# Kernel tuning notes

Hardware: AMD Instinct MI355X
Metric: run time of the kernel (lower is better)

## Reference

```python
import jax, jax.numpy as jnp
import numpy as np

DIM = 2048
N_HEADS = 32
N_KV_HEADS = 8
HEAD_DIM = DIM // N_HEADS
B, T = 2, 2048


def setup_inputs() -> dict:
    key = jax.random.key(0)
    ks = jax.random.split(key, 5)
    std = 0.02
    return {
        "x": jax.random.normal(ks[0], (B, T, DIM), dtype=jnp.float32),
        "wq": jax.random.normal(ks[1], (DIM, DIM), dtype=jnp.float32) * std,
        "wk": jax.random.normal(ks[2], (N_KV_HEADS * HEAD_DIM, DIM), dtype=jnp.float32) * std,
        "wv": jax.random.normal(ks[3], (N_KV_HEADS * HEAD_DIM, DIM), dtype=jnp.float32) * std,
        "wo": jax.random.normal(ks[4], (DIM, DIM), dtype=jnp.float32) * std,
    }


def _rope_tables(seq_len, head_dim, dtype):
    inv_freq = 1.0 / (10000.0 ** (jnp.arange(0, head_dim, 2, dtype=jnp.float32) / head_dim))
    t = jnp.arange(seq_len, dtype=jnp.float32)
    freqs = jnp.einsum("i,j->ij", t, inv_freq)          # [T, hd/2]
    emb = jnp.concatenate([freqs, freqs], axis=-1)       # [T, hd]
    return jnp.cos(emb).astype(dtype), jnp.sin(emb).astype(dtype)


def _rotate_half(x):
    h = x.shape[-1] // 2
    return jnp.concatenate([-x[..., h:], x[..., :h]], axis=-1)


def reference(x, wq, wk, wv, wo):
    Bc, Tc, C = x.shape
    q = (x @ wq.T).reshape(Bc, Tc, N_HEADS, HEAD_DIM).transpose(0, 2, 1, 3)      # [B,H,T,hd]
    k = (x @ wk.T).reshape(Bc, Tc, N_KV_HEADS, HEAD_DIM).transpose(0, 2, 1, 3)   # [B,Hk,T,hd]
    v = (x @ wv.T).reshape(Bc, Tc, N_KV_HEADS, HEAD_DIM).transpose(0, 2, 1, 3)

    cos, sin = _rope_tables(Tc, HEAD_DIM, x.dtype)  # [T,hd] broadcast over B,H
    q = q * cos + _rotate_half(q) * sin
    k = k * cos + _rotate_half(k) * sin

    rep = N_HEADS // N_KV_HEADS
    k = jnp.repeat(k, rep, axis=1)  # [B,H,T,hd]
    v = jnp.repeat(v, rep, axis=1)

    scale = 1.0 / np.sqrt(HEAD_DIM)
    scores = jnp.einsum("bhqd,bhkd->bhqk", q, k) * scale   # [B,H,T,T]
    causal = jnp.triu(jnp.ones((Tc, Tc), dtype=bool), k=1)
    scores = jnp.where(causal, jnp.asarray(-jnp.inf, scores.dtype), scores)
    attn = jax.nn.softmax(scores, axis=-1)
    out = jnp.einsum("bhqk,bhkd->bhqd", attn, v)           # [B,H,T,hd]
    out = out.transpose(0, 2, 1, 3).reshape(Bc, Tc, C)
    return out @ wo.T
```

## Files before the change

### kernel.cpp

```cpp
#include <hip/hip_runtime.h>


typedef unsigned short u16;
typedef __attribute__((ext_vector_type(8))) short bf16x8;
typedef __attribute__((ext_vector_type(4))) float f32x4;
typedef __attribute__((ext_vector_type(4))) unsigned short u16x4;

constexpr int T_SEQ = 2048;
constexpr int DIMC  = 2048;
constexpr int NHEAD = 32;
constexpr int HDIM  = 64;
constexpr int KVDIM = 512;
constexpr int BATCH = 2;

__device__ __forceinline__ u16 f2bf(float f) {
    union { float f; unsigned int i; } v; v.f = f;
    unsigned int r = v.i + 0x7FFFu + ((v.i >> 16) & 1u);
    return (u16)(r >> 16);
}

__device__ __forceinline__ unsigned int pack2_bf16(float e0, float e1) {
    return __builtin_amdgcn_perm(__float_as_uint(e1), __float_as_uint(e0),
                                 0x07060302u);
}

typedef __attribute__((address_space(1))) unsigned int as1_uint;
typedef __attribute__((address_space(3))) unsigned int as3_uint;
__device__ __forceinline__ void glds16(const u16* g, u16* l) {
    __builtin_amdgcn_global_load_lds((as1_uint*)(u16*)g, (as3_uint*)l, 16, 0, 0);
}

__global__ __launch_bounds__(256) void cvt5(const float* __restrict__ x,
                                            const float* __restrict__ wq,
                                            const float* __restrict__ wk,
                                            const float* __restrict__ wv,
                                            const float* __restrict__ wo,
                                            u16* __restrict__ xb,  u16* __restrict__ wqb,
                                            u16* __restrict__ wkb, u16* __restrict__ wvb,
                                            u16* __restrict__ wob) {
    constexpr int E0 = BATCH * T_SEQ * DIMC;
    constexpr int E1 = E0 + DIMC * DIMC;
    constexpr int E2 = E1 + KVDIM * DIMC;
    constexpr int E3 = E2 + KVDIM * DIMC;
    constexpr int E4 = E3 + DIMC * DIMC;
    for (int i = (blockIdx.x * 256 + threadIdx.x) * 4; i < E4; i += gridDim.x * 1024) {
        const float* s; u16* d; int off;
        if (i < E0)      { s = x;  d = xb;  off = 0;  }
        else if (i < E1) { s = wq; d = wqb; off = E0; }
        else if (i < E2) { s = wk; d = wkb; off = E1; }
        else if (i < E3) { s = wv; d = wvb; off = E2; }
        else             { s = wo; d = wob; off = E3; }
        f32x4 v = *(const f32x4*)(s + (i - off));
        u16x4 o;
        #pragma unroll
        for (int e = 0; e < 4; ++e) o[e] = f2bf(v[e]);
        *(u16x4*)(d + (i - off)) = o;
    }
}

template <bool OUTF32>
__device__ __forceinline__ void gemm_core(const u16* __restrict__ A,
                                          const u16* __restrict__ W,
                                          void* __restrict__ Cv,
                                          int rowBase, int colBase,
                                          int N, int K, bool rope) {
    __shared__ __align__(16) u16 As[2 * 128 * 32];
    __shared__ __align__(16) u16 Bs[2 * 128 * 32];

    const int tid  = threadIdx.x;
    const int lane = tid & 63;
    const int w    = tid >> 6;
    const int quad = lane >> 4;
    const int ln   = lane & 15;
    const int wm = (w >> 1) * 64;
    const int wn = (w & 1) * 64;

    f32x4 acc[4][4] = {};

    const int srow = lane >> 2;
    const int scol = (lane & 3) * 8;
    const u16* aC0 = A + (size_t)(rowBase + w * 16 + srow) * K + scol;
    const u16* aC1 = A + (size_t)(rowBase + (w + 4) * 16 + srow) * K + scol;
    const u16* bC0 = W + (size_t)(colBase + w * 16 + srow) * K + scol;
    const u16* bC1 = W + (size_t)(colBase + (w + 4) * 16 + srow) * K + scol;
    u16* asl0 = As + w * 512;
    u16* asl1 = As + (w + 4) * 512;
    u16* bsl0 = Bs + w * 512;
    u16* bsl1 = Bs + (w + 4) * 512;

    for (int kk = 0; kk < K; kk += 64) {
        __syncthreads();
        glds16(aC0 + kk, asl0);
        glds16(aC1 + kk, asl1);
        glds16(bC0 + kk, bsl0);
        glds16(bC1 + kk, bsl1);
        glds16(aC0 + kk + 32, asl0 + 4096);
        glds16(aC1 + kk + 32, asl1 + 4096);
        glds16(bC0 + kk + 32, bsl0 + 4096);
        glds16(bC1 + kk + 32, bsl1 + 4096);
        __syncthreads();

        #pragma unroll
        for (int hp = 0; hp < 2; ++hp) {
            const u16* Ap = As + hp * 4096;
            const u16* Bp = Bs + hp * 4096;
            bf16x8 bw[4];
            #pragma unroll
            for (int j = 0; j < 4; ++j)
                bw[j] = *(const bf16x8*)(Bp + (wn + j * 16 + ln) * 32 + quad * 8);
            #pragma unroll
            for (int i = 0; i < 4; ++i) {
                bf16x8 af = *(const bf16x8*)(Ap + (wm + i * 16 + ln) * 32 + quad * 8);
                #pragma unroll
                for (int j = 0; j < 4; ++j)
                    acc[i][j] = __builtin_amdgcn_mfma_f32_16x16x32_bf16(af, bw[j], acc[i][j], 0, 0, 0);
            }
        }
    }

    if (rope) {
        #pragma unroll
        for (int j = 0; j < 2; ++j) {
            const int d = j * 16 + ln;
            const float invrev = exp2f(-(float)d * (13.287712379549449f / 32.0f))
                                 * 0.15915494309189535f;
            #pragma unroll
            for (int i = 0; i < 4; ++i) {
                #pragma unroll
                for (int r = 0; r < 4; ++r) {
                    const int t = (rowBase + wm + i * 16 + quad * 4 + r) & (T_SEQ - 1);
                    float rev = (float)t * invrev;
                    float fr = rev - floorf(rev);
                    float sn = __builtin_amdgcn_sinf(fr);
                    float cs = __builtin_amdgcn_cosf(fr);
                    float a0 = acc[i][j][r], a2 = acc[i][j + 2][r];
                    acc[i][j][r]     = a0 * cs - a2 * sn;
                    acc[i][j + 2][r] = a2 * cs + a0 * sn;
                }
            }
        }
    }

    #pragma unroll
    for (int i = 0; i < 4; ++i) {
        int mrow = rowBase + wm + i * 16 + quad * 4;
        #pragma unroll
        for (int j = 0; j < 4; ++j) {
            int n = colBase + wn + j * 16 + ln;
            #pragma unroll
            for (int r = 0; r < 4; ++r) {
                if constexpr (OUTF32)
                    ((float*)Cv)[(size_t)(mrow + r) * N + n] = acc[i][j][r];
                else
                    ((u16*)Cv)[(size_t)(mrow + r) * N + n] = f2bf(acc[i][j][r]);
            }
        }
    }
}

__global__ __launch_bounds__(256, 4) void qkv_gemm(const u16* __restrict__ xb,
                                                   const u16* __restrict__ wqb,
                                                   const u16* __restrict__ wkb,
                                                   const u16* __restrict__ wvb,
                                                   u16* __restrict__ Qb,
                                                   u16* __restrict__ Kb,
                                                   u16* __restrict__ Vb) {
    const int nb = blockIdx.x;
    const int rowBase = blockIdx.y * 128;
    const u16* W; u16* C; int colBase, N; bool rope;
    if (nb < 16)      { W = wqb; C = Qb; colBase = nb * 128;        N = DIMC;  rope = true; }
    else if (nb < 20) { W = wkb; C = Kb; colBase = (nb - 16) * 128; N = KVDIM; rope = true; }
    else              { W = wvb; C = Vb; colBase = (nb - 20) * 128; N = KVDIM; rope = false; }
    gemm_core<false>(xb, W, C, rowBase, colBase, N, DIMC, rope);
}

__global__ __launch_bounds__(256, 4) void gemm_out64(const u16* __restrict__ A,
                                                     const u16* __restrict__ W,
                                                     float* __restrict__ C) {
    __shared__ __align__(16) u16 As[2 * 128 * 32];
    __shared__ __align__(16) u16 Bs[2 * 64 * 32];

    const int tid  = threadIdx.x;
    const int lane = tid & 63;
    const int w    = tid >> 6;
    const int quad = lane >> 4;
    const int ln   = lane & 15;
    const int rowBase = blockIdx.y * 128;
    const int colBase = blockIdx.x * 64;
    const int wm = w * 32;
    constexpr int K = DIMC, N = DIMC;

    f32x4 acc[2][4] = {};

    const int srow = lane >> 2;
    const int scol = (lane & 3) * 8;
    const u16* aC0 = A + (size_t)(rowBase + w * 16 + srow) * K + scol;
    const u16* aC1 = A + (size_t)(rowBase + (w + 4) * 16 + srow) * K + scol;
    const u16* bC  = W + (size_t)(colBase + w * 16 + srow) * K + scol;
    u16* asl0 = As + w * 512;
    u16* asl1 = As + (w + 4) * 512;
    u16* bsl  = Bs + w * 512;

    for (int kk = 0; kk < K; kk += 64) {
        __syncthreads();
        glds16(aC0 + kk, asl0);
        glds16(aC1 + kk, asl1);
        glds16(bC  + kk, bsl);
        glds16(aC0 + kk + 32, asl0 + 4096);
        glds16(aC1 + kk + 32, asl1 + 4096);
        glds16(bC  + kk + 32, bsl + 2048);
        __syncthreads();

        #pragma unroll
        for (int hp = 0; hp < 2; ++hp) {
            const u16* Ap = As + hp * 4096;
            const u16* Bp = Bs + hp * 2048;
            bf16x8 bw[4];
            #pragma unroll
            for (int j = 0; j < 4; ++j)
                bw[j] = *(const bf16x8*)(Bp + (j * 16 + ln) * 32 + quad * 8);
            #pragma unroll
            for (int i = 0; i < 2; ++i) {
                bf16x8 af = *(const bf16x8*)(Ap + (wm + i * 16 + ln) * 32 + quad * 8);
                #pragma unroll
                for (int j = 0; j < 4; ++j)
                    acc[i][j] = __builtin_amdgcn_mfma_f32_16x16x32_bf16(af, bw[j], acc[i][j], 0, 0, 0);
            }
        }
    }

    #pragma unroll
    for (int i = 0; i < 2; ++i) {
        int mrow = rowBase + wm + i * 16 + quad * 4;
        #pragma unroll
        for (int j = 0; j < 4; ++j) {
            int n = colBase + j * 16 + ln;
            #pragma unroll
            for (int r = 0; r < 4; ++r)
                C[(size_t)(mrow + r) * N + n] = acc[i][j][r];
        }
    }
}

__global__ __launch_bounds__(256) void transpose_v(const u16* __restrict__ V,
                                                   u16* __restrict__ Vt) {
    __shared__ __align__(16) u16 tile[32][33];
    const int x = threadIdx.x & 31;
    const int y = threadIdx.x >> 5;
    const int tok0 = blockIdx.y * 32;
    const int c0   = blockIdx.x * 32;
    #pragma unroll
    for (int yy = 0; yy < 32; yy += 8)
        tile[y + yy][x] = V[(size_t)(tok0 + y + yy) * KVDIM + c0 + x];
    __syncthreads();
    const int b  = tok0 >> 11;
    const int t0 = tok0 & (T_SEQ - 1);
    #pragma unroll
    for (int yy = 0; yy < 32; yy += 8)
        Vt[(size_t)(b * KVDIM + c0 + y + yy) * T_SEQ + t0 + x] = tile[x][y + yy];
}

__global__ __launch_bounds__(256) void attn(const u16* __restrict__ Q,
                                            const u16* __restrict__ Kx,
                                            const u16* __restrict__ Vt,
                                            u16* __restrict__ O) {
    __shared__ __align__(16) u16 Ks[64][72];
    __shared__ __align__(16) u16 Vs[64][72];

    const int tid  = threadIdx.x;
    const int lane = tid & 63;
    const int w    = tid >> 6;
    const int quad = lane >> 4;
    const int ln   = lane & 15;
    const int h    = blockIdx.y;
    const int b    = blockIdx.z;
    const int kvh  = h >> 2;

    const int srow = tid >> 2;
    const int c    = tid & 3;
    const int scol = c * 16;
    const int vsb  = 32 * (c >> 1) + 4 * (c & 1);
    const u16* kbase = Kx + (size_t)(b * T_SEQ + srow) * KVDIM + kvh * HDIM + scol;
    const u16* vbase = Vt + (size_t)(b * KVDIM + kvh * HDIM + srow) * T_SEQ;

    const float K1 = 0.125f * 1.4426950408889634f;
    const float K2 = 8.0f * 1.4426950408889634f;

    #pragma unroll
    for (int phase = 0; phase < 2; ++phase) {
        const int qt = phase ? (31 - (int)blockIdx.x) : (int)blockIdx.x;
        const int qr0 = qt * 64 + w * 16;

        const u16* qp = Q + (size_t)(b * T_SEQ + qr0 + ln) * DIMC + h * HDIM + quad * 8;
        const bf16x8 bq0 = *(const bf16x8*)qp;
        const bf16x8 bq1 = *(const bf16x8*)(qp + 32);

        f32x4 o[4] = {};
        float lsum = 0.0f;

        for (int kt = 0; kt <= qt; ++kt) {
            const int k0 = kt * 64;
            __syncthreads();
            *(bf16x8*)&Ks[srow][scol]     = *(const bf16x8*)(kbase + (size_t)k0 * KVDIM);
            *(bf16x8*)&Ks[srow][scol + 8] = *(const bf16x8*)(kbase + (size_t)k0 * KVDIM + 8);
            {
                union { bf16x8 v; u16x4 h4[2]; } va, vb;
                va.v = *(const bf16x8*)(vbase + k0 + scol);
                vb.v = *(const bf16x8*)(vbase + k0 + scol + 8);
                *(u16x4*)&Vs[srow][vsb]      = va.h4[0];
                *(u16x4*)&Vs[srow][vsb + 8]  = va.h4[1];
                *(u16x4*)&Vs[srow][vsb + 16] = vb.h4[0];
                *(u16x4*)&Vs[srow][vsb + 24] = vb.h4[1];
            }
            __syncthreads();

            f32x4 s[4];
            #pragma unroll
            for (int st = 0; st < 4; ++st) {
                f32x4 z = {};
                s[st] = __builtin_amdgcn_mfma_f32_16x16x32_bf16(
                            *(const bf16x8*)&Ks[st * 16 + ln][quad * 8], bq0, z, 0, 0, 0);
                s[st] = __builtin_amdgcn_mfma_f32_16x16x32_bf16(
                            *(const bf16x8*)&Ks[st * 16 + ln][32 + quad * 8], bq1, s[st], 0, 0, 0);
            }

            unsigned int pk[8];
            if (kt != qt) {
                #pragma unroll
                for (int st = 0; st < 4; ++st) {
                    float e0 = exp2f(fmaf(s[st][0], K1, -K2));
                    float e1 = exp2f(fmaf(s[st][1], K1, -K2));
                    float e2 = exp2f(fmaf(s[st][2], K1, -K2));
                    float e3 = exp2f(fmaf(s[st][3], K1, -K2));
                    lsum += (e0 + e1) + (e2 + e3);
                    pk[2 * st]     = pack2_bf16(e0, e1);
                    pk[2 * st + 1] = pack2_bf16(e2, e3);
                }
            } else {
                const int thr = w * 16 + ln;
                #pragma unroll
                for (int st = 0; st < 4; ++st) {
                    float e[4];
                    #pragma unroll
                    for (int r = 0; r < 4; ++r) {
                        const int key = st * 16 + quad * 4 + r;
                        e[r] = (key > thr) ? 0.0f : exp2f(fmaf(s[st][r], K1, -K2));
                    }
                    lsum += (e[0] + e[1]) + (e[2] + e[3]);
                    pk[2 * st]     = pack2_bf16(e[0], e[1]);
                    pk[2 * st + 1] = pack2_bf16(e[2], e[3]);
                }
            }

            union { unsigned int u[4]; bf16x8 v; } a0, a1;
            a0.u[0] = pk[0]; a0.u[1] = pk[1]; a0.u[2] = pk[2]; a0.u[3] = pk[3];
            a1.u[0] = pk[4]; a1.u[1] = pk[5]; a1.u[2] = pk[6]; a1.u[3] = pk[7];

            #pragma unroll
            for (int t = 0; t < 4; ++t) {
                o[t] = __builtin_amdgcn_mfma_f32_16x16x32_bf16(
                           a0.v, *(const bf16x8*)&Vs[t * 16 + ln][quad * 8], o[t], 0, 0, 0);
                o[t] = __builtin_amdgcn_mfma_f32_16x16x32_bf16(
                           a1.v, *(const bf16x8*)&Vs[t * 16 + ln][32 + quad * 8], o[t], 0, 0, 0);
            }
        }

        float ls = lsum;
        ls += __shfl_xor(ls, 16);
        ls += __shfl_xor(ls, 32);
        #pragma unroll
        for (int r = 0; r < 4; ++r) {
            const float inv = 1.0f / __shfl(ls, quad * 4 + r);
            size_t obase = (size_t)(b * T_SEQ + qr0 + quad * 4 + r) * DIMC + h * HDIM;
            #pragma unroll
            for (int t = 0; t < 4; ++t)
                O[obase + t * 16 + ln] = f2bf(o[t][r] * inv);
        }
    }
}

extern "C" void kernel_launch(void* const* d_in, const int* in_sizes, int n_in,
                              void* d_out, int out_size, void* d_ws, size_t ws_size,
                              hipStream_t stream) {
    const float* x  = (const float*)d_in[0];
    const float* wq = (const float*)d_in[1];
    const float* wk = (const float*)d_in[2];
    const float* wv = (const float*)d_in[3];
    const float* wo = (const float*)d_in[4];
    float* out = (float*)d_out;

    char* ws = (char*)d_ws;
    constexpr size_t MB = 1024 * 1024;
    u16* Qb  = (u16*)(ws);
    u16* Kb  = (u16*)(ws + 16 * MB);
    u16* Vb  = (u16*)(ws + 20 * MB);
    u16* Vtb = (u16*)(ws + 24 * MB);
    u16* AOb = (u16*)(ws + 28 * MB);
    u16* xb  = AOb;
    u16* wqb = (u16*)(ws + 44 * MB);
    u16* wkb = (u16*)(ws + 52 * MB);
    u16* wvb = (u16*)(ws + 54 * MB);
    u16* wob = (u16*)(ws + 56 * MB);
    const int M = BATCH * T_SEQ;

    hipLaunchKernelGGL(cvt5, dim3(2048), dim3(256), 0, stream,
                       x, wq, wk, wv, wo, xb, wqb, wkb, wvb, wob);
    hipLaunchKernelGGL(qkv_gemm, dim3(24, M / 128), dim3(256), 0, stream,
                       xb, wqb, wkb, wvb, Qb, Kb, Vb);
    hipLaunchKernelGGL(transpose_v, dim3(KVDIM / 32, M / 32), dim3(256), 0, stream, Vb, Vtb);
    hipLaunchKernelGGL(attn, dim3(16, NHEAD, BATCH), dim3(256), 0, stream,
                       Qb, Kb, Vtb, AOb);
    hipLaunchKernelGGL(gemm_out64, dim3(DIMC / 64, M / 128), dim3(256), 0, stream,
                       AOb, wob, out);
}
```

Before: 316.7 us.

## Prefetch next K/V tile into registers and raise wave priority around MFMA

The attention loop now loads the next K and V tile from global memory into registers while the current tile is being computed, then writes them to shared memory at the start of the next iteration. The second __syncthreads is replaced by an explicit lgkmcnt wait plus s_barrier, so the barrier does not wait on the outstanding global prefetch loads. It also wraps the MFMA blocks in s_setprio to favour matrix issue. The goal is to hide global load latency behind compute, at the cost of extra VGPRs, which may reduce occupancy.

```diff
diff --git a/kernel.cpp b/kernel.cpp
--- a/kernel.cpp
+++ b/kernel.cpp
@@ -298,23 +298,38 @@
         f32x4 o[4] = {};
         float lsum = 0.0f;
 
+        bf16x8 kra = *(const bf16x8*)kbase;
+        bf16x8 krb = *(const bf16x8*)(kbase + 8);
+        bf16x8 vra = *(const bf16x8*)(vbase + scol);
+        bf16x8 vrb = *(const bf16x8*)(vbase + scol + 8);
+
         for (int kt = 0; kt <= qt; ++kt) {
-            const int k0 = kt * 64;
             __syncthreads();
-            *(bf16x8*)&Ks[srow][scol]     = *(const bf16x8*)(kbase + (size_t)k0 * KVDIM);
-            *(bf16x8*)&Ks[srow][scol + 8] = *(const bf16x8*)(kbase + (size_t)k0 * KVDIM + 8);
+
+            *(bf16x8*)&Ks[srow][scol]     = kra;
+            *(bf16x8*)&Ks[srow][scol + 8] = krb;
             {
-                union { bf16x8 v; u16x4 h4[2]; } va, vb;
-                va.v = *(const bf16x8*)(vbase + k0 + scol);
-                vb.v = *(const bf16x8*)(vbase + k0 + scol + 8);
-                *(u16x4*)&Vs[srow][vsb]      = va.h4[0];
-                *(u16x4*)&Vs[srow][vsb + 8]  = va.h4[1];
-                *(u16x4*)&Vs[srow][vsb + 16] = vb.h4[0];
-                *(u16x4*)&Vs[srow][vsb + 24] = vb.h4[1];
-            }
-            __syncthreads();
+                union { bf16x8 v; u16x4 h4[2]; } ua, ub;
+                ua.v = vra; ub.v = vrb;
+                *(u16x4*)&Vs[srow][vsb]      = ua.h4[0];
+                *(u16x4*)&Vs[srow][vsb + 8]  = ua.h4[1];
+                *(u16x4*)&Vs[srow][vsb + 16] = ub.h4[0];
+                *(u16x4*)&Vs[srow][vsb + 24] = ub.h4[1];
+            }
+
+            if (kt < qt) {
+                const size_t ko = (size_t)(kt + 1) * 64;
+                kra = *(const bf16x8*)(kbase + ko * KVDIM);
+                krb = *(const bf16x8*)(kbase + ko * KVDIM + 8);
+                vra = *(const bf16x8*)(vbase + ko + scol);
+                vrb = *(const bf16x8*)(vbase + ko + scol + 8);
+            }
+
+            __asm__ __volatile__("s_waitcnt lgkmcnt(0)" ::: "memory");
+            __builtin_amdgcn_s_barrier();
 
             f32x4 s[4];
+            __builtin_amdgcn_s_setprio(1);
             #pragma unroll
             for (int st = 0; st < 4; ++st) {
                 f32x4 z = {};
@@ -323,6 +338,7 @@
                 s[st] = __builtin_amdgcn_mfma_f32_16x16x32_bf16(
                             *(const bf16x8*)&Ks[st * 16 + ln][32 + quad * 8], bq1, s[st], 0, 0, 0);
             }
+            __builtin_amdgcn_s_setprio(0);
 
             unsigned int pk[8];
             if (kt != qt) {
@@ -356,6 +372,7 @@
             a0.u[0] = pk[0]; a0.u[1] = pk[1]; a0.u[2] = pk[2]; a0.u[3] = pk[3];
             a1.u[0] = pk[4]; a1.u[1] = pk[5]; a1.u[2] = pk[6]; a1.u[3] = pk[7];
 
+            __builtin_amdgcn_s_setprio(1);
             #pragma unroll
             for (int t = 0; t < 4; ++t) {
                 o[t] = __builtin_amdgcn_mfma_f32_16x16x32_bf16(
@@ -363,6 +380,7 @@
                 o[t] = __builtin_amdgcn_mfma_f32_16x16x32_bf16(
                            a1.v, *(const bf16x8*)&Vs[t * 16 + ln][32 + quad * 8], o[t], 0, 0, 0);
             }
+            __builtin_amdgcn_s_setprio(0);
         }
 
         float ls = lsum;
```

Measured after the change: 304.5 us. -3.9%, faster.
